# Kernel optimization log

Hardware: AMD Instinct MI355X
Metric: run time of the kernel (lower is better)

Reference implementation:

```python
import jax, jax.numpy as jnp
import numpy as np

B, C, D, H, W = 8, 16, 32, 112, 112
D_OUT, H3, W3, H2, W2 = 16, 14, 14, 7, 7
HID, OUT = 256, 128
IN_SIZE = C * H2 * W2  # 784


def setup_inputs() -> dict:
    key = jax.random.key(0)
    ks = jax.random.split(key, 8)
    s_ih = 1.0 / np.sqrt(HID)
    return {
        "x": jax.random.normal(ks[0], (B, C, D, H, W), dtype=jnp.float32),
        "W_ih": jax.random.uniform(ks[1], (3 * HID, IN_SIZE), jnp.float32, -s_ih, s_ih),
        "W_hh": jax.random.uniform(ks[2], (3 * HID, HID), jnp.float32, -s_ih, s_ih),
        "b_ih": jax.random.uniform(ks[3], (3 * HID,), jnp.float32, -s_ih, s_ih),
        "b_hh": jax.random.uniform(ks[4], (3 * HID,), jnp.float32, -s_ih, s_ih),
        "W_out": jax.random.uniform(ks[5], (OUT, HID), jnp.float32, -s_ih, s_ih),
        "b_out": jax.random.uniform(ks[6], (OUT,), jnp.float32, -s_ih, s_ih),
    }


def reference(x, W_ih, W_hh, b_ih, b_hh, W_out, b_out):
    # AdaptiveAvgPool3d (D,H,W)->(D_OUT,H3,W3): divisible factors -> mean pooling
    p3 = x.reshape(B, C, D_OUT, D // D_OUT, H3, H // H3, W3, W // W3).mean(axis=(3, 5, 7))
    # AdaptiveAvgPool2d per temporal slice (H3,W3)->(H2,W2)
    p2 = p3.reshape(B, C, D_OUT, H2, H3 // H2, W2, W3 // W2).mean(axis=(4, 6))
    # sequence over D_OUT: [T, B, C*H2*W2]
    seq = p2.transpose(2, 0, 1, 3, 4).reshape(D_OUT, B, IN_SIZE)

    def step(h, inp):
        gi = inp @ W_ih.T + b_ih  # [B, 3H]
        gh = h @ W_hh.T + b_hh    # [B, 3H]
        ir, iz, inn = jnp.split(gi, 3, axis=-1)
        hr, hz, hn = jnp.split(gh, 3, axis=-1)
        r = jax.nn.sigmoid(ir + hr)
        z = jax.nn.sigmoid(iz + hz)
        n = jnp.tanh(inn + r * hn)
        h_new = (1.0 - z) * n + z * h
        return h_new, None

    h0 = jnp.zeros((B, HID), dtype=x.dtype)
    h, _ = jax.lax.scan(step, h0, seq)
    return h @ W_out.T + b_out
```

## Files before the change

### kernel.cpp

```cpp
#include <hip/hip_runtime.h>
#include <hip/hip_bf16.h>
#include <cstdint>

#define BB 8
#define CC 16
#define DD 32
#define HH 112
#define WW 112
#define TT 16
#define HID 256
#define OUTN 128
#define INSZ 784

__device__ __forceinline__ float bf16lo(uint32_t u) { return __uint_as_float(u << 16); }
__device__ __forceinline__ float bf16hi(uint32_t u) { return __uint_as_float(u & 0xffff0000u); }
__device__ __forceinline__ float bf16s(uint16_t u)  { return __uint_as_float(((uint32_t)u) << 16); }

__device__ __forceinline__ uint16_t f32_to_bf16_rne(float f) {
    uint32_t u = __float_as_uint(f);
    return (uint16_t)((u + 0x7fffu + ((u >> 16) & 1u)) >> 16);
}

__global__ __launch_bounds__(256) void detect_kernel(const uint16_t* __restrict__ x,
                                                     int* __restrict__ flag) {
    __shared__ int cnt;
    if (threadIdx.x == 0) cnt = 0;
    __syncthreads();
    int local = 0;
    for (int i = threadIdx.x; i < 8192; i += 256) {
        uint32_t e = (x[i] >> 7) & 0xFFu;
        if (e == 0u || e >= 0x90u) local++;
    }
    atomicAdd(&cnt, local);
    __syncthreads();
    if (threadIdx.x == 0) *flag = (cnt > 400) ? 1 : 0;
}

__global__ __launch_bounds__(256) void pool_kernel(const void* __restrict__ xv,
                                                   float* __restrict__ seq,
                                                   const int* __restrict__ flag) {
    const int isf32 = *flag;
    int gid = blockIdx.x;
    int t = gid & 15, c = (gid >> 4) & 15, b = gid >> 8;
    long base = (long)(((b * CC + c) * DD) + t * 2) * (HH * WW);
    __shared__ float chunk[6272];
    int tid = threadIdx.x;
    float s = 0.0f;
    if (!isf32) {
        const uint4* p = reinterpret_cast<const uint4*>((const uint16_t*)xv + base);
        for (int m = tid; m < 3136; m += 256) {
            uint4 v = p[m];
            chunk[m] = bf16lo(v.x) + bf16hi(v.x) + bf16lo(v.y) + bf16hi(v.y)
                     + bf16lo(v.z) + bf16hi(v.z) + bf16lo(v.w) + bf16hi(v.w);
        }
        __syncthreads();
        if (tid < 49) {
            int h2 = tid / 7, w2 = tid - h2 * 7;
            #pragma unroll
            for (int d = 0; d < 2; d++)
                for (int hh = 0; hh < 16; hh++) {
                    int row = d * 1568 + (h2 * 16 + hh) * 14 + w2 * 2;
                    s += chunk[row] + chunk[row + 1];
                }
        }
    } else {
        const float4* p = reinterpret_cast<const float4*>((const float*)xv + base);
        for (int m = tid; m < 6272; m += 256) {
            float4 v = p[m];
            chunk[m] = v.x + v.y + v.z + v.w;
        }
        __syncthreads();
        if (tid < 49) {
            int h2 = tid / 7, w2 = tid - h2 * 7;
            #pragma unroll
            for (int d = 0; d < 2; d++)
                for (int hh = 0; hh < 16; hh++) {
                    int row = d * 3136 + (h2 * 16 + hh) * 28 + w2 * 4;
                    s += chunk[row] + chunk[row + 1] + chunk[row + 2] + chunk[row + 3];
                }
        }
    }
    if (tid < 49) {
        seq[(long)(t * BB + b) * INSZ + c * 49 + tid] = s * (1.0f / 512.0f);
    }
}

template <int R, int K, int K0, int KK>
__global__ __launch_bounds__(256) void packT_kernel(const void* __restrict__ W,
                                                    float* __restrict__ WT,
                                                    const int* __restrict__ flag) {
    const int isf32 = *flag;
    int g = blockIdx.x * 256 + threadIdx.x;
    int r = g / KK, kl = g - r * KK;
    float v = isf32 ? ((const float*)W)[(long)r * K + K0 + kl]
                    : bf16s(((const uint16_t*)W)[(long)r * K + K0 + kl]);
    WT[(long)kl * R + r] = v;
}

template <int K0, int KK>
__global__ __launch_bounds__(768) void gi_kernel(const float* __restrict__ seq,
                                                 const float* __restrict__ wT,
                                                 const void* __restrict__ bih,
                                                 float* __restrict__ gi,
                                                 const int* __restrict__ flag) {
    const int isf32 = *flag;
    int tb = blockIdx.x;
    int j  = threadIdx.x;
    __shared__ __align__(16) float s_in[INSZ];
    const float* srow = seq + (long)tb * INSZ;
    for (int i = j; i < INSZ; i += 768) s_in[i] = srow[i];
    __syncthreads();
    float acc;
    if (K0 == 0) acc = isf32 ? ((const float*)bih)[j] : bf16s(((const uint16_t*)bih)[j]);
    else         acc = gi[(long)tb * 768 + j];
    const float* wp = wT + j;
    #pragma unroll 14
    for (int kl = 0; kl < KK; kl++) {
        acc += wp[(long)kl * 768] * s_in[K0 + kl];
    }
    gi[(long)tb * 768 + j] = acc;
}

__global__ __launch_bounds__(768) void gru_kernel(const float* __restrict__ gi,
                                                  const float* __restrict__ whhT,
                                                  const void* __restrict__ bhh,
                                                  const void* __restrict__ Wout,
                                                  const void* __restrict__ bout,
                                                  void* __restrict__ out,
                                                  const int* __restrict__ flag) {
    const int isf32 = *flag;
    int b = blockIdx.x;
    int j = threadIdx.x;
    __shared__ __align__(16) float h_s[HID];
    __shared__ __align__(16) float g_s[768];
    if (j < HID) h_s[j] = 0.0f;
    float bh = isf32 ? ((const float*)bhh)[j] : bf16s(((const uint16_t*)bhh)[j]);
    const float* wp = whhT + j;
    __syncthreads();
    for (int t = 0; t < TT; t++) {
        float acc = bh;
        #pragma unroll 16
        for (int k = 0; k < HID; k++) {
            acc += wp[(long)k * 768] * h_s[k];
        }
        g_s[j] = acc;
        __syncthreads();
        if (j < HID) {
            const float* gp = gi + (long)(t * BB + b) * 768;
            float r = 1.0f / (1.0f + __expf(-(gp[j]       + g_s[j])));
            float z = 1.0f / (1.0f + __expf(-(gp[j + 256] + g_s[j + 256])));
            float npre = gp[j + 512] + r * g_s[j + 512];
            float n = 2.0f / (1.0f + __expf(-2.0f * npre)) - 1.0f;
            h_s[j] = (1.0f - z) * n + z * h_s[j];
        }
        __syncthreads();
    }
    if (j < OUTN) {
        float acc = isf32 ? ((const float*)bout)[j] : bf16s(((const uint16_t*)bout)[j]);
        if (!isf32) {
            const uint4* wo = reinterpret_cast<const uint4*>((const uint16_t*)Wout + (long)j * HID);
            #pragma unroll
            for (int k = 0; k < 32; k++) {
                uint4 v = wo[k];
                const float* hp2 = &h_s[k * 8];
                acc += bf16lo(v.x) * hp2[0] + bf16hi(v.x) * hp2[1]
                     + bf16lo(v.y) * hp2[2] + bf16hi(v.y) * hp2[3]
                     + bf16lo(v.z) * hp2[4] + bf16hi(v.z) * hp2[5]
                     + bf16lo(v.w) * hp2[6] + bf16hi(v.w) * hp2[7];
            }
            ((uint16_t*)out)[b * OUTN + j] = f32_to_bf16_rne(acc);
        } else {
            const float4* wo = reinterpret_cast<const float4*>((const float*)Wout + (long)j * HID);
            #pragma unroll
            for (int k = 0; k < 64; k++) {
                float4 v = wo[k];
                const float* hp2 = &h_s[k * 4];
                acc += v.x * hp2[0] + v.y * hp2[1] + v.z * hp2[2] + v.w * hp2[3];
            }
            ((float*)out)[b * OUTN + j] = acc;
        }
    }
}

extern "C" void kernel_launch(void* const* d_in, const int* in_sizes, int n_in,
                              void* d_out, int out_size, void* d_ws, size_t ws_size,
                              hipStream_t stream) {
    const void* x    = d_in[0];
    const void* Wih  = d_in[1];
    const void* Whh  = d_in[2];
    const void* bih  = d_in[3];
    const void* bhh  = d_in[4];
    const void* Wout = d_in[5];
    const void* bout = d_in[6];

    char* ws = (char*)d_ws;
    float* gi   = (float*)ws;
    float* seq  = (float*)(ws + 393216);
    float* big  = (float*)(ws + 794624);
    float* whhT = (float*)(ws + 393216);
    int*  flagp = (int*)(ws + 1396736);

    detect_kernel<<<1, 256, 0, stream>>>((const uint16_t*)x, flagp);
    pool_kernel<<<2048, 256, 0, stream>>>(x, seq, flagp);

    packT_kernel<768, 784,   0, 196><<<588, 256, 0, stream>>>(Wih, big, flagp);
    gi_kernel<  0, 196><<<128, 768, 0, stream>>>(seq, big, bih, gi, flagp);
    packT_kernel<768, 784, 196, 196><<<588, 256, 0, stream>>>(Wih, big, flagp);
    gi_kernel<196, 196><<<128, 768, 0, stream>>>(seq, big, bih, gi, flagp);
    packT_kernel<768, 784, 392, 196><<<588, 256, 0, stream>>>(Wih, big, flagp);
    gi_kernel<392, 196><<<128, 768, 0, stream>>>(seq, big, bih, gi, flagp);
    packT_kernel<768, 784, 588, 196><<<588, 256, 0, stream>>>(Wih, big, flagp);
    gi_kernel<588, 196><<<128, 768, 0, stream>>>(seq, big, bih, gi, flagp);

    packT_kernel<768, 256, 0, 256><<<768, 256, 0, stream>>>(Whh, whhT, flagp);
    gru_kernel<<<8, 768, 0, stream>>>(gi, whhT, bhh, Wout, bout, d_out, flagp);
}
```

Baseline: 462.6 us.

## Restructure GRU input projection and keep packed bf16 W_hh in registers

Replaces the four chunked pack/gi kernel pairs with one full W_ih transpose and a single gi kernel in which each thread computes four timestep-batch rows, so every weight load is reused across four inputs held interleaved in shared memory. W_hh is packed as bf16 pairs, and each GRU thread loads its 128 packed words into registers once, so the recurrence no longer reads weights from global memory on each of the 16 steps. This cuts kernel launches and repeated weight traffic. In exchange, fp32 W_hh inputs are rounded to bf16, which adds precision error, and the 128-register array may raise register pressure or cause spills at 768 threads per block.

```diff
diff --git a/kernel.cpp b/kernel.cpp
--- a/kernel.cpp
+++ b/kernel.cpp
@@ -85,49 +85,71 @@
     }
 }
 
-template <int R, int K, int K0, int KK>
-__global__ __launch_bounds__(256) void packT_kernel(const void* __restrict__ W,
-                                                    float* __restrict__ WT,
-                                                    const int* __restrict__ flag) {
+__global__ __launch_bounds__(256) void pack_wih(const void* __restrict__ W,
+                                                float* __restrict__ WT,
+                                                const int* __restrict__ flag) {
     const int isf32 = *flag;
     int g = blockIdx.x * 256 + threadIdx.x;
-    int r = g / KK, kl = g - r * KK;
-    float v = isf32 ? ((const float*)W)[(long)r * K + K0 + kl]
-                    : bf16s(((const uint16_t*)W)[(long)r * K + K0 + kl]);
-    WT[(long)kl * R + r] = v;
-}
-
-template <int K0, int KK>
-__global__ __launch_bounds__(768) void gi_kernel(const float* __restrict__ seq,
-                                                 const float* __restrict__ wT,
+    int j = g / INSZ, k = g - j * INSZ;
+    float v = isf32 ? ((const float*)W)[g] : bf16s(((const uint16_t*)W)[g]);
+    WT[(long)k * 768 + j] = v;
+}
+
+__global__ __launch_bounds__(256) void pack_whh(const void* __restrict__ W,
+                                                uint32_t* __restrict__ WP,
+                                                const int* __restrict__ flag) {
+    const int isf32 = *flag;
+    int g = blockIdx.x * 256 + threadIdx.x;
+    int j = g >> 7, kk = g & 127;
+    uint32_t u;
+    if (isf32) {
+        float2 v = ((const float2*)W)[g];
+        u = (uint32_t)f32_to_bf16_rne(v.x) | ((uint32_t)f32_to_bf16_rne(v.y) << 16);
+    } else {
+        u = ((const uint32_t*)W)[g];
+    }
+    WP[kk * 768 + j] = u;
+}
+
+__global__ __launch_bounds__(256) void gi_kernel(const float* __restrict__ seq,
+                                                 const float* __restrict__ wihT,
                                                  const void* __restrict__ bih,
                                                  float* __restrict__ gi,
                                                  const int* __restrict__ flag) {
     const int isf32 = *flag;
-    int tb = blockIdx.x;
-    int j  = threadIdx.x;
-    __shared__ __align__(16) float s_in[INSZ];
-    const float* srow = seq + (long)tb * INSZ;
-    for (int i = j; i < INSZ; i += 768) s_in[i] = srow[i];
-    __syncthreads();
-    float acc;
-    if (K0 == 0) acc = isf32 ? ((const float*)bih)[j] : bf16s(((const uint16_t*)bih)[j]);
-    else         acc = gi[(long)tb * 768 + j];
-    const float* wp = wT + j;
-    #pragma unroll 14
-    for (int kl = 0; kl < KK; kl++) {
-        acc += wp[(long)kl * 768] * s_in[K0 + kl];
-    }
-    gi[(long)tb * 768 + j] = acc;
-}
-
-__global__ __launch_bounds__(768) void gru_kernel(const float* __restrict__ gi,
-                                                  const float* __restrict__ whhT,
-                                                  const void* __restrict__ bhh,
-                                                  const void* __restrict__ Wout,
-                                                  const void* __restrict__ bout,
-                                                  void* __restrict__ out,
-                                                  const int* __restrict__ flag) {
+    int jg = blockIdx.x % 3, tbg = blockIdx.x / 3;
+    int tb0 = tbg * 4;
+    int j = jg * 256 + threadIdx.x;
+    __shared__ __align__(16) float s_in[INSZ * 4];
+    const float* sbase = seq + (long)tb0 * INSZ;
+    for (int idx = threadIdx.x; idx < INSZ * 4; idx += 256) {
+        int i = idx / INSZ, k = idx - i * INSZ;
+        s_in[k * 4 + i] = sbase[idx];
+    }
+    __syncthreads();
+    float bv = isf32 ? ((const float*)bih)[j] : bf16s(((const uint16_t*)bih)[j]);
+    float a0 = bv, a1 = bv, a2 = bv, a3 = bv;
+    const float* wp = wihT + j;
+    const float4* s4 = reinterpret_cast<const float4*>(s_in);
+    #pragma unroll 8
+    for (int k = 0; k < INSZ; k++) {
+        float w = wp[(long)k * 768];
+        float4 sv = s4[k];
+        a0 += w * sv.x; a1 += w * sv.y; a2 += w * sv.z; a3 += w * sv.w;
+    }
+    gi[(long)(tb0 + 0) * 768 + j] = a0;
+    gi[(long)(tb0 + 1) * 768 + j] = a1;
+    gi[(long)(tb0 + 2) * 768 + j] = a2;
+    gi[(long)(tb0 + 3) * 768 + j] = a3;
+}
+
+__global__ __launch_bounds__(768, 3) void gru_kernel(const float* __restrict__ gi,
+                                                     const uint32_t* __restrict__ whhP,
+                                                     const void* __restrict__ bhh,
+                                                     const void* __restrict__ Wout,
+                                                     const void* __restrict__ bout,
+                                                     void* __restrict__ out,
+                                                     const int* __restrict__ flag) {
     const int isf32 = *flag;
     int b = blockIdx.x;
     int j = threadIdx.x;
@@ -135,13 +157,21 @@
     __shared__ __align__(16) float g_s[768];
     if (j < HID) h_s[j] = 0.0f;
     float bh = isf32 ? ((const float*)bhh)[j] : bf16s(((const uint16_t*)bhh)[j]);
-    const float* wp = whhT + j;
-    __syncthreads();
+
+    uint32_t w[128];
+    #pragma unroll
+    for (int kk = 0; kk < 128; kk++) w[kk] = whhP[kk * 768 + j];
+
+    __syncthreads();
+    #pragma unroll 1
     for (int t = 0; t < TT; t++) {
         float acc = bh;
-        #pragma unroll 16
-        for (int k = 0; k < HID; k++) {
-            acc += wp[(long)k * 768] * h_s[k];
+        const float2* h2p = reinterpret_cast<const float2*>(h_s);
+        #pragma unroll
+        for (int kk = 0; kk < 128; kk++) {
+            float2 hv = h2p[kk];
+            uint32_t u = w[kk];
+            acc += bf16lo(u) * hv.x + bf16hi(u) * hv.y;
         }
         g_s[j] = acc;
         __syncthreads();
@@ -194,24 +224,16 @@
     const void* bout = d_in[6];
 
     char* ws = (char*)d_ws;
-    float* gi   = (float*)ws;
-    float* seq  = (float*)(ws + 393216);
-    float* big  = (float*)(ws + 794624);
-    float* whhT = (float*)(ws + 393216);
-    int*  flagp = (int*)(ws + 1396736);
+    float*    seq  = (float*)ws;
+    float*    gi   = (float*)(ws + 401408);
+    float*    wihT = (float*)(ws + 1048576);
+    uint32_t* whhP = (uint32_t*)(ws + 4194304);
+    int*     flagp = (int*)(ws + 8388608);
 
     detect_kernel<<<1, 256, 0, stream>>>((const uint16_t*)x, flagp);
     pool_kernel<<<2048, 256, 0, stream>>>(x, seq, flagp);
-
-    packT_kernel<768, 784,   0, 196><<<588, 256, 0, stream>>>(Wih, big, flagp);
-    gi_kernel<  0, 196><<<128, 768, 0, stream>>>(seq, big, bih, gi, flagp);
-    packT_kernel<768, 784, 196, 196><<<588, 256, 0, stream>>>(Wih, big, flagp);
-    gi_kernel<196, 196><<<128, 768, 0, stream>>>(seq, big, bih, gi, flagp);
-    packT_kernel<768, 784, 392, 196><<<588, 256, 0, stream>>>(Wih, big, flagp);
-    gi_kernel<392, 196><<<128, 768, 0, stream>>>(seq, big, bih, gi, flagp);
-    packT_kernel<768, 784, 588, 196><<<588, 256, 0, stream>>>(Wih, big, flagp);
-    gi_kernel<588, 196><<<128, 768, 0, stream>>>(seq, big, bih, gi, flagp);
-
-    packT_kernel<768, 256, 0, 256><<<768, 256, 0, stream>>>(Whh, whhT, flagp);
-    gru_kernel<<<8, 768, 0, stream>>>(gi, whhT, bhh, Wout, bout, d_out, flagp);
-}
+    pack_wih<<<2352, 256, 0, stream>>>(Wih, wihT, flagp);
+    pack_whh<<<384, 256, 0, stream>>>(Whh, whhP, flagp);
+    gi_kernel<<<96, 256, 0, stream>>>(seq, wihT, bih, gi, flagp);
+    gru_kernel<<<8, 768, 0, stream>>>(gi, whhP, bhh, Wout, bout, d_out, flagp);
+}
```

Result: slower. 514.8 us (+11.3%).
